# Kernel tuning notes

Hardware: AMD Instinct MI355X
Metric: run time of the kernel (lower is better)

## Reference

```python
import jax, jax.numpy as jnp
import numpy as np

B, T, C = 2, 4096, 768
H = 12
D = C // H  # head_dim = 64


def setup_inputs() -> dict:
    key = jax.random.key(0)
    k1, k2, k3 = jax.random.split(key, 3)
    x = jax.random.normal(k1, (B, T, C), dtype=jnp.float32)
    Wqkv = jax.random.normal(k2, (C, 3 * C), dtype=jnp.float32) * (C ** -0.5)
    Wproj = jax.random.normal(k3, (C, C), dtype=jnp.float32) * (C ** -0.5)
    bproj = jnp.zeros((C,), dtype=jnp.float32)
    return {"x": x, "Wqkv": Wqkv, "Wproj": Wproj, "bproj": bproj}


def reference(x, Wqkv, Wproj, bproj):
    b, t, c = x.shape
    # qkv projection (no bias), split into heads: [3, B, H, T, D]
    qkv = (x @ Wqkv).reshape(b, t, 3, H, D).transpose(2, 0, 3, 1, 4)
    q, k, v = qkv[0], qkv[1], qkv[2]
    scale = D ** -0.5
    # full causal score matrix [B, H, T, T] (faithful to naive impl)
    scores = jnp.einsum('bhqd,bhkd->bhqk', q, k) * scale
    causal = jnp.tril(jnp.ones((t, t), dtype=bool))
    scores = jnp.where(causal[None, None], scores, -jnp.inf)
    attn = jax.nn.softmax(scores, axis=-1)
    out = jnp.einsum('bhqk,bhkd->bhqd', attn, v)
    out = out.transpose(0, 2, 1, 3).reshape(b, t, c)
    return out @ Wproj + bproj
```

## Files before the change

kernel.cpp:

```cpp
#include <hip/hip_runtime.h>

#define B_ 2
#define T_ 4096
#define C_ 768
#define H_ 12
#define D_ 64
#define QTASK 96

typedef __attribute__((ext_vector_type(8))) short bf16x8;
typedef __attribute__((ext_vector_type(4))) float f32x4;
typedef __attribute__((ext_vector_type(16))) float f32x16;

__device__ __forceinline__ unsigned short f2bf(float f) {
  union { float f; unsigned u; } v; v.f = f;
  unsigned r = v.u + 0x7fffu + ((v.u >> 16) & 1u);
  return (unsigned short)(r >> 16);
}

__device__ __forceinline__ float exp2_hw(float x) {
  float r;
  asm("v_exp_f32 %0, %1" : "=v"(r) : "v"(x));
  return r;
}

__device__ __forceinline__ void gll16(const void* g, void* l) {
  __builtin_amdgcn_global_load_lds((const __attribute__((address_space(1))) void*)g,
                                   (__attribute__((address_space(3))) void*)l, 16, 0, 0);
}


__global__ __launch_bounds__(256) void cast_bf16_k(const float* __restrict__ in,
                                                   unsigned short* __restrict__ out, int n4,
                                                   unsigned* __restrict__ cnt) {
  int i = blockIdx.x * 256 + threadIdx.x;
  if (i < 128) cnt[i] = 0u;
  if (i >= n4) return;
  float4 v = ((const float4*)in)[i];
  union { unsigned short s[4]; unsigned long long u; } o;
  o.s[0] = f2bf(v.x); o.s[1] = f2bf(v.y); o.s[2] = f2bf(v.z); o.s[3] = f2bf(v.w);
  ((unsigned long long*)out)[i] = o.u;
}

__global__ __launch_bounds__(256) void tpose2_k(const float* __restrict__ a,
                                                unsigned short* __restrict__ ao,
                                                const float* __restrict__ b,
                                                unsigned short* __restrict__ bo) {
  __shared__ unsigned short t[64][65];
  int id = blockIdx.x;
  const float* in; unsigned short* out; int R, C, bx, by;
  if (id < 432) { in = a; out = ao; R = 768; C = 2304; bx = id % 36; by = id / 36; }
  else { id -= 432; in = b; out = bo; R = 768; C = 768; bx = id % 12; by = id / 12; }
  const int c0 = bx * 64, r0 = by * 64;
  const int tr = threadIdx.x >> 6, tc = threadIdx.x & 63;
#pragma unroll
  for (int i = 0; i < 16; ++i) {
    int r = i * 4 + tr;
    t[r][tc] = f2bf(in[(size_t)(r0 + r) * C + c0 + tc]);
  }
  __syncthreads();
#pragma unroll
  for (int i = 0; i < 16; ++i) {
    int c = i * 4 + tr;
    out[(size_t)(c0 + c) * R + r0 + tc] = t[tc][c];
  }
}


#define QSCALE 0.1803368801111243f

__global__ __launch_bounds__(256) void gemm_k(const unsigned short* __restrict__ A,
                                              const unsigned short* __restrict__ Bt,
                                              int K,
                                              unsigned short* __restrict__ q_out,
                                              unsigned short* __restrict__ k_out,
                                              unsigned short* __restrict__ vt_out) {
  __shared__ short a_lds[2][128 * 32];
  __shared__ short b_lds[2][128 * 32];
  const int tid = threadIdx.x;
  const int wave = tid >> 6, lane = tid & 63;
  const int wm = wave >> 1, wn = wave & 1;
  const int lr = lane & 15, lc = lane >> 4;

  const int id = blockIdx.x;
  const int xcd = id & 7, idc = id >> 3;
  const int bx = xcd * 8 + (idc & 7);
  const int by = idc >> 3;
  const int m0 = bx * 128, n0 = by * 128;

  f32x4 acc[4][4];
  for (int mi = 0; mi < 4; ++mi)
    for (int ni = 0; ni < 4; ++ni) acc[mi][ni] = (f32x4){0.f, 0.f, 0.f, 0.f};

  const unsigned short *ap[2], *bp[2];
  int lb[2];
#pragma unroll
  for (int p = 0; p < 2; ++p) {
    int chunk = p * 256 + wave * 64 + lane;
    int r = chunk >> 2, cc = chunk & 3;
    int c = cc ^ ((r >> 1) & 3);
    ap[p] = A + (size_t)(m0 + r) * K + c * 8;
    bp[p] = Bt + (size_t)(n0 + r) * K + c * 8;
    lb[p] = (p * 256 + wave * 64) * 8;
  }

  const int nks = K >> 5;
#pragma unroll
  for (int p = 0; p < 2; ++p) {
    gll16(ap[p], &a_lds[0][lb[p]]);
    gll16(bp[p], &b_lds[0][lb[p]]);
    ap[p] += 32; bp[p] += 32;
  }

  for (int ks = 0; ks < nks; ++ks) {
    const int buf = ks & 1;
    __builtin_amdgcn_s_barrier();
    __builtin_amdgcn_sched_barrier(0);
    if (ks + 1 < nks) {
#pragma unroll
      for (int p = 0; p < 2; ++p) {
        gll16(ap[p], &a_lds[buf ^ 1][lb[p]]);
        gll16(bp[p], &b_lds[buf ^ 1][lb[p]]);
        ap[p] += 32; bp[p] += 32;
      }
      asm volatile("s_waitcnt vmcnt(4)" ::: "memory");
    } else {
      asm volatile("s_waitcnt vmcnt(0)" ::: "memory");
    }
    __builtin_amdgcn_sched_barrier(0);
    __builtin_amdgcn_s_barrier();
    __builtin_amdgcn_sched_barrier(0);

    bf16x8 af[4], bfrag[4];
#pragma unroll
    for (int mi = 0; mi < 4; ++mi) {
      int r = wm * 64 + mi * 16 + lr;
      af[mi] = *(const bf16x8*)&a_lds[buf][r * 32 + (lc ^ ((r >> 1) & 3)) * 8];
    }
#pragma unroll
    for (int ni = 0; ni < 4; ++ni) {
      int r = wn * 64 + ni * 16 + lr;
      bfrag[ni] = *(const bf16x8*)&b_lds[buf][r * 32 + (lc ^ ((r >> 1) & 3)) * 8];
    }
    __builtin_amdgcn_s_setprio(1);
#pragma unroll
    for (int mi = 0; mi < 4; ++mi)
#pragma unroll
      for (int ni = 0; ni < 4; ++ni)
        acc[mi][ni] = __builtin_amdgcn_mfma_f32_16x16x32_bf16(af[mi], bfrag[ni], acc[mi][ni], 0, 0, 0);
    __builtin_amdgcn_s_setprio(0);
  }

  const int nn0 = n0 + wn * 64 + lr;
  const int which = n0 / 768;
#pragma unroll
  for (int mi = 0; mi < 4; ++mi)
#pragma unroll
    for (int ni = 0; ni < 4; ++ni) {
      int nn = nn0 + ni * 16;
      int rem = nn - which * 768;
      int h = rem >> 6, d = rem & 63;
      int t0v = m0 + wm * 64 + mi * 16 + lc * 4;
      int b = t0v >> 12, t = t0v & (T_ - 1);
      size_t bh = (size_t)(b * H_ + h);
      if (which == 2) {
        unsigned u0, u1;
        asm("v_cvt_pk_bf16_f32 %0, %1, %2" : "=v"(u0) : "v"(acc[mi][ni][0]), "v"(acc[mi][ni][1]));
        asm("v_cvt_pk_bf16_f32 %0, %1, %2" : "=v"(u1) : "v"(acc[mi][ni][2]), "v"(acc[mi][ni][3]));
        uint2 u = {u0, u1};
        *(uint2*)&vt_out[(bh * D_ + d) * T_ + t] = u;
      } else {
#pragma unroll
        for (int r = 0; r < 4; ++r) {
          float av = acc[mi][ni][r];
          if (which == 0) av *= QSCALE;
          unsigned short val = f2bf(av);
          if (which == 0) q_out[(bh * T_ + t + r) * D_ + d] = val;
          else            k_out[(bh * T_ + t + r) * D_ + d] = val;
        }
      }
    }
}


__global__ __launch_bounds__(256) void gemm2_k(const unsigned short* __restrict__ A,
                                               const unsigned short* __restrict__ Bt,
                                               float* __restrict__ f_out,
                                               const float* __restrict__ bias) {
  __shared__ short a_lds[2][64 * 32];
  __shared__ short b_lds[2][128 * 32];
  const int tid = threadIdx.x;
  const int wave = tid >> 6, lane = tid & 63;
  const int wm = wave >> 1, wn = wave & 1;
  const int lr = lane & 15, lc = lane >> 4;
  const int K = C_;

  const int id = blockIdx.x;
  const int xcd = id & 7, idc = id >> 3;
  const int bx = xcd * 16 + (idc & 15);
  const int by = idc >> 4;
  const int m0 = bx * 64, n0 = by * 128;

  f32x4 acc[2][4];
  for (int mi = 0; mi < 2; ++mi)
    for (int ni = 0; ni < 4; ++ni) acc[mi][ni] = (f32x4){0.f, 0.f, 0.f, 0.f};

  const unsigned short *apt, *bpt[2];
  int lba, lbb[2];
  {
    int chunk = wave * 64 + lane;
    int r = chunk >> 2, cc = chunk & 3;
    int c = cc ^ ((r >> 1) & 3);
    apt = A + (size_t)(m0 + r) * K + c * 8;
    lba = (wave * 64) * 8;
  }
#pragma unroll
  for (int p = 0; p < 2; ++p) {
    int chunk = p * 256 + wave * 64 + lane;
    int r = chunk >> 2, cc = chunk & 3;
    int c = cc ^ ((r >> 1) & 3);
    bpt[p] = Bt + (size_t)(n0 + r) * K + c * 8;
    lbb[p] = (p * 256 + wave * 64) * 8;
  }

  const int nks = K >> 5;
  gll16(apt, &a_lds[0][lba]); apt += 32;
#pragma unroll
  for (int p = 0; p < 2; ++p) { gll16(bpt[p], &b_lds[0][lbb[p]]); bpt[p] += 32; }

  for (int ks = 0; ks < nks; ++ks) {
    const int buf = ks & 1;
    __builtin_amdgcn_s_barrier();
    __builtin_amdgcn_sched_barrier(0);
    if (ks + 1 < nks) {
      gll16(apt, &a_lds[buf ^ 1][lba]); apt += 32;
#pragma unroll
      for (int p = 0; p < 2; ++p) { gll16(bpt[p], &b_lds[buf ^ 1][lbb[p]]); bpt[p] += 32; }
      asm volatile("s_waitcnt vmcnt(3)" ::: "memory");
    } else {
      asm volatile("s_waitcnt vmcnt(0)" ::: "memory");
    }
    __builtin_amdgcn_sched_barrier(0);
    __builtin_amdgcn_s_barrier();
    __builtin_amdgcn_sched_barrier(0);

    bf16x8 af[2], bfrag[4];
#pragma unroll
    for (int mi = 0; mi < 2; ++mi) {
      int r = wm * 32 + mi * 16 + lr;
      af[mi] = *(const bf16x8*)&a_lds[buf][r * 32 + (lc ^ ((r >> 1) & 3)) * 8];
    }
#pragma unroll
    for (int ni = 0; ni < 4; ++ni) {
      int r = wn * 64 + ni * 16 + lr;
      bfrag[ni] = *(const bf16x8*)&b_lds[buf][r * 32 + (lc ^ ((r >> 1) & 3)) * 8];
    }
    __builtin_amdgcn_s_setprio(1);
#pragma unroll
    for (int mi = 0; mi < 2; ++mi)
#pragma unroll
      for (int ni = 0; ni < 4; ++ni)
        acc[mi][ni] = __builtin_amdgcn_mfma_f32_16x16x32_bf16(af[mi], bfrag[ni], acc[mi][ni], 0, 0, 0);
    __builtin_amdgcn_s_setprio(0);
  }

#pragma unroll
  for (int mi = 0; mi < 2; ++mi)
#pragma unroll
    for (int ni = 0; ni < 4; ++ni) {
      int nn = n0 + wn * 64 + ni * 16 + lr;
      float bv = bias[nn];
#pragma unroll
      for (int r = 0; r < 4; ++r) {
        int m = m0 + wm * 32 + mi * 16 + lc * 4 + r;
        f_out[(size_t)m * C_ + nn] = acc[mi][ni][r] + bv;
      }
    }
}


#define PACK8(SV, O)                                                              \
  do {                                                                            \
    unsigned w0, w1, w2, w3, w4, w5, w6, w7;                                      \
    asm("v_cvt_pk_bf16_f32 %0, %1, %2" : "=v"(w0) : "v"(SV[0]), "v"(SV[1]));      \
    asm("v_cvt_pk_bf16_f32 %0, %1, %2" : "=v"(w1) : "v"(SV[2]), "v"(SV[3]));      \
    asm("v_cvt_pk_bf16_f32 %0, %1, %2" : "=v"(w2) : "v"(SV[4]), "v"(SV[5]));      \
    asm("v_cvt_pk_bf16_f32 %0, %1, %2" : "=v"(w3) : "v"(SV[6]), "v"(SV[7]));      \
    asm("v_cvt_pk_bf16_f32 %0, %1, %2" : "=v"(w4) : "v"(SV[8]), "v"(SV[9]));      \
    asm("v_cvt_pk_bf16_f32 %0, %1, %2" : "=v"(w5) : "v"(SV[10]), "v"(SV[11]));    \
    asm("v_cvt_pk_bf16_f32 %0, %1, %2" : "=v"(w6) : "v"(SV[12]), "v"(SV[13]));    \
    asm("v_cvt_pk_bf16_f32 %0, %1, %2" : "=v"(w7) : "v"(SV[14]), "v"(SV[15]));    \
    asm("v_permlane32_swap_b32 %0, %1" : "+v"(w0), "+v"(w2));                     \
    asm("v_permlane32_swap_b32 %0, %1" : "+v"(w1), "+v"(w3));                     \
    asm("v_permlane32_swap_b32 %0, %1" : "+v"(w4), "+v"(w6));                     \
    asm("v_permlane32_swap_b32 %0, %1" : "+v"(w5), "+v"(w7));                     \
    pw[(O) + 0] = w0; pw[(O) + 1] = w1; pw[(O) + 2] = w2; pw[(O) + 3] = w3;       \
    pw[(O) + 4] = w4; pw[(O) + 5] = w5; pw[(O) + 6] = w6; pw[(O) + 7] = w7;       \
  } while (0)

__global__ __launch_bounds__(256) void flash5_k(const unsigned short* __restrict__ Qg,
                                                const unsigned short* __restrict__ Kg,
                                                const unsigned short* __restrict__ Vtg,
                                                unsigned short* __restrict__ Og,
                                                unsigned* __restrict__ cnt) {
  __shared__ short k_lds[2][8 * 512];
  __shared__ short vt_lds[2][8 * 512];
  __shared__ int task_s;

  const int tid = threadIdx.x;
  const int wave = tid >> 6, lane = tid & 63;
  const int lq = lane & 31, hi = lane >> 5;
  const int xq = blockIdx.x & 7;
  unsigned* myq = cnt + xq * 16;

  for (;;) {
    if (tid == 0) task_s = (int)atomicAdd(myq, 1u);
    __syncthreads();
    const int task = task_s;
    if (task >= QTASK) return;

    const int qi = 31 - task / 3;
    const int bh = xq * 3 + (task - (task / 3) * 3);
    const int qw = qi * 128 + wave * 32;
    const int q_g = qw + lq;

    const size_t kbase = (size_t)bh * T_ * D_;
    const size_t vbase = (size_t)bh * D_ * T_;

    const unsigned short* qrow = Qg + kbase + (size_t)q_g * D_;
    bf16x8 qf[4];
#pragma unroll
    for (int t = 0; t < 4; ++t) qf[t] = *(const bf16x8*)(qrow + t * 16 + hi * 8);

    f32x16 accT0, accT1;
#pragma unroll
    for (int r = 0; r < 16; ++r) { accT0[r] = 0.f; accT1[r] = 0.f; }
    float lvec[16];
#pragma unroll
    for (int r = 0; r < 16; ++r) lvec[r] = 0.f;
    float m = 0.f;

    const int nt = 2 * qi + 2;

    const unsigned short* kp = Kg + kbase + (size_t)((wave & 1) * 32 + lq) * D_ + (wave >> 1) * 16 + hi * 8;
    const unsigned short* vp = Vtg + vbase + (size_t)((wave & 1) * 32 + lq) * T_ + (wave >> 1) * 16 + hi * 8;
    const int lb0 = wave * 512, lb1 = (wave + 4) * 512;

    gll16(kp, &k_lds[0][lb0]); gll16(kp + 32, &k_lds[0][lb1]);
    gll16(vp, &vt_lds[0][lb0]); gll16(vp + 32, &vt_lds[0][lb1]);
    const unsigned short* kpn = kp + 64 * D_;
    const unsigned short* vpn = vp + 64;

    for (int it = 0; it < nt; ++it) {
      const int kv = it * 64;
      const int buf = it & 1;

      __builtin_amdgcn_s_barrier();
      __builtin_amdgcn_sched_barrier(0);
      if (it + 1 < nt) {
        gll16(kpn, &k_lds[buf ^ 1][lb0]); gll16(kpn + 32, &k_lds[buf ^ 1][lb1]);
        gll16(vpn, &vt_lds[buf ^ 1][lb0]); gll16(vpn + 32, &vt_lds[buf ^ 1][lb1]);
        kpn += 64 * D_; vpn += 64;
        asm volatile("s_waitcnt vmcnt(4)" ::: "memory");
      } else {
        asm volatile("s_waitcnt vmcnt(0)" ::: "memory");
      }
      __builtin_amdgcn_sched_barrier(0);
      __builtin_amdgcn_s_barrier();
      __builtin_amdgcn_sched_barrier(0);

      if (kv <= qw + 31) {
        const float negm = -m;
        f32x16 s0, s1;
#pragma unroll
        for (int r = 0; r < 16; ++r) { s0[r] = negm; s1[r] = negm; }
        __builtin_amdgcn_s_setprio(1);
#pragma unroll
        for (int t = 0; t < 4; ++t) {
          bf16x8 kf0 = *(const bf16x8*)&k_lds[buf][(t * 2 + 0) * 512 + lane * 8];
          bf16x8 kf1 = *(const bf16x8*)&k_lds[buf][(t * 2 + 1) * 512 + lane * 8];
          s0 = __builtin_amdgcn_mfma_f32_32x32x16_bf16(kf0, qf[t], s0, 0, 0, 0);
          s1 = __builtin_amdgcn_mfma_f32_32x32x16_bf16(kf1, qf[t], s1, 0, 0, 0);
        }
        __builtin_amdgcn_s_setprio(0);

        if (kv + 63 > qw) {
#pragma unroll
          for (int r = 0; r < 16; ++r) {
            int key0 = kv + ((r & 3) + 8 * (r >> 2) + 4 * hi);
            if (key0 > q_g) s0[r] = -INFINITY;
            if (key0 + 32 > q_g) s1[r] = -INFINITY;
          }
        }

        float mx[16];
#pragma unroll
        for (int r = 0; r < 16; ++r) mx[r] = fmaxf(s0[r], s1[r]);
        float a0 = fmaxf(fmaxf(mx[0], mx[1]), mx[2]);
        float a1 = fmaxf(fmaxf(mx[3], mx[4]), mx[5]);
        float a2 = fmaxf(fmaxf(mx[6], mx[7]), mx[8]);
        float a3 = fmaxf(fmaxf(mx[9], mx[10]), mx[11]);
        float a4 = fmaxf(fmaxf(mx[12], mx[13]), mx[14]);
        float rx = fmaxf(fmaxf(fmaxf(a0, a1), fmaxf(a2, a3)), fmaxf(a4, mx[15]));
        rx = fmaxf(rx, __shfl_xor(rx, 32));

        if (!__all(rx <= 8.f)) {
          float dlt = fmaxf(rx, 0.f);
          float al = exp2_hw(-dlt);
          m += dlt;
#pragma unroll
          for (int r = 0; r < 16; ++r) { accT0[r] *= al; accT1[r] *= al; lvec[r] *= al; }
#pragma unroll
          for (int r = 0; r < 16; ++r) { s0[r] -= dlt; s1[r] -= dlt; }
        }
#pragma unroll
        for (int r = 0; r < 16; ++r) s0[r] = exp2_hw(s0[r]);
#pragma unroll
        for (int r = 0; r < 16; ++r) s1[r] = exp2_hw(s1[r]);
#pragma unroll
        for (int r = 0; r < 16; ++r) lvec[r] += s0[r] + s1[r];

        unsigned pw[16];
        PACK8(s0, 0);
        PACK8(s1, 8);

        __builtin_amdgcn_s_setprio(1);
#pragma unroll
        for (int ks = 0; ks < 4; ++ks) {
          union { unsigned u[4]; bf16x8 v; } pb;
          pb.u[0] = pw[ks * 4 + 0]; pb.u[1] = pw[ks * 4 + 1];
          pb.u[2] = pw[ks * 4 + 2]; pb.u[3] = pw[ks * 4 + 3];
          bf16x8 vf0 = *(const bf16x8*)&vt_lds[buf][(ks * 2 + 0) * 512 + lane * 8];
          bf16x8 vf1 = *(const bf16x8*)&vt_lds[buf][(ks * 2 + 1) * 512 + lane * 8];
          accT0 = __builtin_amdgcn_mfma_f32_32x32x16_bf16(vf0, pb.v, accT0, 0, 0, 0);
          accT1 = __builtin_amdgcn_mfma_f32_32x32x16_bf16(vf1, pb.v, accT1, 0, 0, 0);
        }
        __builtin_amdgcn_s_setprio(0);
      }
    }

    float l = 0.f;
#pragma unroll
    for (int r = 0; r < 16; ++r) l += lvec[r];
    l += __shfl_xor(l, 32);
    const float inv = 1.0f / l;
    const int b = bh / H_, h = bh - b * H_;
    unsigned short* orow = Og + ((size_t)b * T_ + q_g) * C_ + h * D_;
#pragma unroll
    for (int g = 0; g < 4; ++g) {
      int d0 = 8 * g + 4 * hi;
      float e0 = accT0[4 * g + 0] * inv, e1 = accT0[4 * g + 1] * inv;
      float e2 = accT0[4 * g + 2] * inv, e3 = accT0[4 * g + 3] * inv;
      float f0 = accT1[4 * g + 0] * inv, f1 = accT1[4 * g + 1] * inv;
      float f2 = accT1[4 * g + 2] * inv, f3 = accT1[4 * g + 3] * inv;
      uint2 ua, ub;
      asm("v_cvt_pk_bf16_f32 %0, %1, %2" : "=v"(ua.x) : "v"(e0), "v"(e1));
      asm("v_cvt_pk_bf16_f32 %0, %1, %2" : "=v"(ua.y) : "v"(e2), "v"(e3));
      asm("v_cvt_pk_bf16_f32 %0, %1, %2" : "=v"(ub.x) : "v"(f0), "v"(f1));
      asm("v_cvt_pk_bf16_f32 %0, %1, %2" : "=v"(ub.y) : "v"(f2), "v"(f3));
      *(uint2*)(orow + d0) = ua;
      *(uint2*)(orow + 32 + d0) = ub;
    }
    __syncthreads();
  }
}


extern "C" void kernel_launch(void* const* d_in, const int* in_sizes, int n_in,
                              void* d_out, int out_size, void* d_ws, size_t ws_size,
                              hipStream_t stream) {
  const float* x     = (const float*)d_in[0];
  const float* Wqkv  = (const float*)d_in[1];
  const float* Wproj = (const float*)d_in[2];
  const float* bproj = (const float*)d_in[3];
  float* out = (float*)d_out;

  char* ws = (char*)d_ws;
  unsigned short* xbf   = (unsigned short*)(ws);
  unsigned short* wqkvt = (unsigned short*)(ws + 12582912);
  unsigned short* wprjt = (unsigned short*)(ws + 16121856);
  unsigned short* Qb    = (unsigned short*)(ws + 17301504);
  unsigned short* Kb    = (unsigned short*)(ws + 29884416);
  unsigned short* Vtb   = (unsigned short*)(ws + 42467328);
  unsigned*       cnt   = (unsigned*)(ws + 55050240);

  cast_bf16_k<<<6144, 256, 0, stream>>>(x, xbf, (B_ * T_ * C_) / 4, cnt);
  tpose2_k<<<576, 256, 0, stream>>>(Wqkv, wqkvt, Wproj, wprjt);

  gemm_k<<<(B_ * T_ / 128) * (3 * C_ / 128), 256, 0, stream>>>(
      xbf, wqkvt, C_, Qb, Kb, Vtb);

  flash5_k<<<1024, 256, 0, stream>>>(Qb, Kb, Vtb, xbf, cnt);

  gemm2_k<<<(B_ * T_ / 64) * (C_ / 128), 256, 0, stream>>>(xbf, wprjt, out, bproj);
}
```

Baseline: 194.1 us.

## Split long causal query tiles across KV halves with separate merge kernel

```diff
diff --git a/kernel.cpp b/kernel.cpp
--- a/kernel.cpp
+++ b/kernel.cpp
@@ -5,7 +5,7 @@
 #define C_ 768
 #define H_ 12
 #define D_ 64
-#define QTASK 96
+#define QTASK 144
 
 typedef __attribute__((ext_vector_type(8))) short bf16x8;
 typedef __attribute__((ext_vector_type(4))) float f32x4;
@@ -277,6 +277,25 @@
     }
 }
 
+__device__ const unsigned char g_tasktbl[48] = {
+  15, 0x80|31, 0xC0|31,
+      0x80|30, 0xC0|30,
+  14, 0x80|29, 0xC0|29,
+      0x80|28, 0xC0|28,
+  13, 0x80|27, 0xC0|27,
+      0x80|26, 0xC0|26,
+  12, 0x80|25, 0xC0|25,
+      0x80|24, 0xC0|24,
+  11, 0x80|23, 0xC0|23,
+      0x80|22, 0xC0|22,
+  10, 0x80|21, 0xC0|21,
+      0x80|20, 0xC0|20,
+   9, 0x80|19, 0xC0|19,
+      0x80|18, 0xC0|18,
+   8, 0x80|17, 0xC0|17,
+      0x80|16, 0xC0|16,
+   7, 6, 5, 4, 3, 2, 1, 0
+};
 
 #define PACK8(SV, O)                                                              \
   do {                                                                            \
@@ -297,11 +316,12 @@
     pw[(O) + 4] = w4; pw[(O) + 5] = w5; pw[(O) + 6] = w6; pw[(O) + 7] = w7;       \
   } while (0)
 
-__global__ __launch_bounds__(256) void flash5_k(const unsigned short* __restrict__ Qg,
-                                                const unsigned short* __restrict__ Kg,
-                                                const unsigned short* __restrict__ Vtg,
-                                                unsigned short* __restrict__ Og,
-                                                unsigned* __restrict__ cnt) {
+__global__ __launch_bounds__(256) void flash14_k(const unsigned short* __restrict__ Qg,
+                                                 const unsigned short* __restrict__ Kg,
+                                                 const unsigned short* __restrict__ Vtg,
+                                                 unsigned short* __restrict__ Og,
+                                                 unsigned* __restrict__ cnt,
+                                                 unsigned short* __restrict__ part) {
   __shared__ short k_lds[2][8 * 512];
   __shared__ short vt_lds[2][8 * 512];
   __shared__ int task_s;
@@ -318,11 +338,19 @@
     const int task = task_s;
     if (task >= QTASK) return;
 
-    const int qi = 31 - task / 3;
-    const int bh = xq * 3 + (task - (task / 3) * 3);
+    const int d3 = task / 3;
+    const int desc = g_tasktbl[d3];
+    const int qi = desc & 63;
+    const int split = desc >> 7;
+    const int half = (desc >> 6) & 1;
+    const int bh = xq * 3 + (task - d3 * 3);
     const int qw = qi * 128 + wave * 32;
     const int q_g = qw + lq;
 
+    const int it0 = (split && half) ? (qi + 1) : 0;
+    const int itN = split ? (half ? (2 * qi + 2) : (qi + 1)) : (2 * qi + 2);
+    const int ntl = itN - it0;
+
     const size_t kbase = (size_t)bh * T_ * D_;
     const size_t vbase = (size_t)bh * D_ * T_;
 
@@ -339,10 +367,10 @@
     for (int r = 0; r < 16; ++r) lvec[r] = 0.f;
     float m = 0.f;
 
-    const int nt = 2 * qi + 2;
-
-    const unsigned short* kp = Kg + kbase + (size_t)((wave & 1) * 32 + lq) * D_ + (wave >> 1) * 16 + hi * 8;
-    const unsigned short* vp = Vtg + vbase + (size_t)((wave & 1) * 32 + lq) * T_ + (wave >> 1) * 16 + hi * 8;
+    const unsigned short* kp = Kg + kbase + (size_t)((wave & 1) * 32 + lq) * D_ +
+                               (wave >> 1) * 16 + hi * 8 + (size_t)it0 * 64 * D_;
+    const unsigned short* vp = Vtg + vbase + (size_t)((wave & 1) * 32 + lq) * T_ +
+                               (wave >> 1) * 16 + hi * 8 + it0 * 64;
     const int lb0 = wave * 512, lb1 = (wave + 4) * 512;
 
     gll16(kp, &k_lds[0][lb0]); gll16(kp + 32, &k_lds[0][lb1]);
@@ -350,13 +378,13 @@
     const unsigned short* kpn = kp + 64 * D_;
     const unsigned short* vpn = vp + 64;
 
-    for (int it = 0; it < nt; ++it) {
-      const int kv = it * 64;
-      const int buf = it & 1;
+    for (int j = 0; j < ntl; ++j) {
+      const int kv = (it0 + j) * 64;
+      const int buf = j & 1;
 
       __builtin_amdgcn_s_barrier();
       __builtin_amdgcn_sched_barrier(0);
-      if (it + 1 < nt) {
+      if (j + 1 < ntl) {
         gll16(kpn, &k_lds[buf ^ 1][lb0]); gll16(kpn + 32, &k_lds[buf ^ 1][lb1]);
         gll16(vpn, &vt_lds[buf ^ 1][lb0]); gll16(vpn + 32, &vt_lds[buf ^ 1][lb1]);
         kpn += 64 * D_; vpn += 64;
@@ -442,25 +470,101 @@
 #pragma unroll
     for (int r = 0; r < 16; ++r) l += lvec[r];
     l += __shfl_xor(l, 32);
-    const float inv = 1.0f / l;
-    const int b = bh / H_, h = bh - b * H_;
-    unsigned short* orow = Og + ((size_t)b * T_ + q_g) * C_ + h * D_;
-#pragma unroll
-    for (int g = 0; g < 4; ++g) {
-      int d0 = 8 * g + 4 * hi;
-      float e0 = accT0[4 * g + 0] * inv, e1 = accT0[4 * g + 1] * inv;
-      float e2 = accT0[4 * g + 2] * inv, e3 = accT0[4 * g + 3] * inv;
-      float f0 = accT1[4 * g + 0] * inv, f1 = accT1[4 * g + 1] * inv;
-      float f2 = accT1[4 * g + 2] * inv, f3 = accT1[4 * g + 3] * inv;
-      uint2 ua, ub;
-      asm("v_cvt_pk_bf16_f32 %0, %1, %2" : "=v"(ua.x) : "v"(e0), "v"(e1));
-      asm("v_cvt_pk_bf16_f32 %0, %1, %2" : "=v"(ua.y) : "v"(e2), "v"(e3));
-      asm("v_cvt_pk_bf16_f32 %0, %1, %2" : "=v"(ub.x) : "v"(f0), "v"(f1));
-      asm("v_cvt_pk_bf16_f32 %0, %1, %2" : "=v"(ub.y) : "v"(f2), "v"(f3));
-      *(uint2*)(orow + d0) = ua;
-      *(uint2*)(orow + 32 + d0) = ub;
+
+    if (!split) {
+      const float inv = 1.0f / l;
+      const int b = bh / H_, h = bh - b * H_;
+      unsigned short* orow = Og + ((size_t)b * T_ + q_g) * C_ + h * D_;
+#pragma unroll
+      for (int g = 0; g < 4; ++g) {
+        int d0 = 8 * g + 4 * hi;
+        float e0 = accT0[4 * g + 0] * inv, e1 = accT0[4 * g + 1] * inv;
+        float e2 = accT0[4 * g + 2] * inv, e3 = accT0[4 * g + 3] * inv;
+        float f0 = accT1[4 * g + 0] * inv, f1 = accT1[4 * g + 1] * inv;
+        float f2 = accT1[4 * g + 2] * inv, f3 = accT1[4 * g + 3] * inv;
+        uint2 ua, ub;
+        asm("v_cvt_pk_bf16_f32 %0, %1, %2" : "=v"(ua.x) : "v"(e0), "v"(e1));
+        asm("v_cvt_pk_bf16_f32 %0, %1, %2" : "=v"(ua.y) : "v"(e2), "v"(e3));
+        asm("v_cvt_pk_bf16_f32 %0, %1, %2" : "=v"(ub.x) : "v"(f0), "v"(f1));
+        asm("v_cvt_pk_bf16_f32 %0, %1, %2" : "=v"(ub.y) : "v"(f2), "v"(f3));
+        *(uint2*)(orow + d0) = ua;
+        *(uint2*)(orow + 32 + d0) = ub;
+      }
+    } else {
+      unsigned short* pbase = part + (size_t)((bh * 16 + (qi - 16)) * 2 + half) * 9216;
+      unsigned w[16];
+#pragma unroll
+      for (int g = 0; g < 8; ++g)
+        asm("v_cvt_pk_bf16_f32 %0, %1, %2" : "=v"(w[g]) : "v"(accT0[2 * g]), "v"(accT0[2 * g + 1]));
+#pragma unroll
+      for (int g = 0; g < 8; ++g)
+        asm("v_cvt_pk_bf16_f32 %0, %1, %2" : "=v"(w[8 + g]) : "v"(accT1[2 * g]), "v"(accT1[2 * g + 1]));
+      uint4* po = (uint4*)(pbase + tid * 32);
+#pragma unroll
+      for (int g = 0; g < 4; ++g) {
+        uint4 u = {w[4 * g + 0], w[4 * g + 1], w[4 * g + 2], w[4 * g + 3]};
+        po[g] = u;
+      }
+      float2 ml = {m, l};
+      ((float2*)(pbase + 8192))[tid] = ml;
     }
     __syncthreads();
+  }
+}
+
+__global__ __launch_bounds__(256) void merge_k(const unsigned short* __restrict__ part,
+                                               unsigned short* __restrict__ Og) {
+  const int slot = blockIdx.x;
+  const int bh = slot >> 4, qi = (slot & 15) + 16;
+  const int tid = threadIdx.x;
+  const int wave = tid >> 6, lane = tid & 63;
+  const int lq = lane & 31, hi = lane >> 5;
+
+  const unsigned short* pa = part + (size_t)(slot * 2 + 0) * 9216;
+  const unsigned short* pb = part + (size_t)(slot * 2 + 1) * 9216;
+  float2 mla = ((const float2*)(pa + 8192))[tid];
+  float2 mlb = ((const float2*)(pb + 8192))[tid];
+  float newm = fmaxf(mla.x, mlb.x);
+  float sa = exp2_hw(mla.x - newm), sb = exp2_hw(mlb.x - newm);
+  float l = mla.y * sa + mlb.y * sb;
+  float inv = 1.0f / l;
+
+  const uint4* qa = (const uint4*)(pa + tid * 32);
+  const uint4* qb = (const uint4*)(pb + tid * 32);
+  float o[32];
+#pragma unroll
+  for (int g = 0; g < 4; ++g) {
+    uint4 ua = qa[g], ub = qb[g];
+#pragma unroll
+    for (int e = 0; e < 4; ++e) {
+      unsigned wa = ((const unsigned*)&ua)[e];
+      unsigned wb = ((const unsigned*)&ub)[e];
+      union { unsigned u; float f; } la_, ha_, lb_, hb_;
+      la_.u = wa << 16; ha_.u = wa & 0xffff0000u;
+      lb_.u = wb << 16; hb_.u = wb & 0xffff0000u;
+      int r = g * 8 + e * 2;
+      o[r]     = la_.f * sa + lb_.f * sb;
+      o[r + 1] = ha_.f * sa + hb_.f * sb;
+    }
+  }
+
+  const int q_g = qi * 128 + wave * 32 + lq;
+  const int b = bh / H_, h = bh - b * H_;
+  unsigned short* orow = Og + ((size_t)b * T_ + q_g) * C_ + h * D_;
+#pragma unroll
+  for (int g = 0; g < 4; ++g) {
+    int d0 = 8 * g + 4 * hi;
+    float e0 = o[4 * g + 0] * inv, e1 = o[4 * g + 1] * inv;
+    float e2 = o[4 * g + 2] * inv, e3 = o[4 * g + 3] * inv;
+    float f0 = o[16 + 4 * g + 0] * inv, f1 = o[16 + 4 * g + 1] * inv;
+    float f2 = o[16 + 4 * g + 2] * inv, f3 = o[16 + 4 * g + 3] * inv;
+    uint2 ua, ub;
+    asm("v_cvt_pk_bf16_f32 %0, %1, %2" : "=v"(ua.x) : "v"(e0), "v"(e1));
+    asm("v_cvt_pk_bf16_f32 %0, %1, %2" : "=v"(ua.y) : "v"(e2), "v"(e3));
+    asm("v_cvt_pk_bf16_f32 %0, %1, %2" : "=v"(ub.x) : "v"(f0), "v"(f1));
+    asm("v_cvt_pk_bf16_f32 %0, %1, %2" : "=v"(ub.y) : "v"(f2), "v"(f3));
+    *(uint2*)(orow + d0) = ua;
+    *(uint2*)(orow + 32 + d0) = ub;
   }
 }
 
@@ -482,6 +586,7 @@
   unsigned short* Kb    = (unsigned short*)(ws + 29884416);
   unsigned short* Vtb   = (unsigned short*)(ws + 42467328);
   unsigned*       cnt   = (unsigned*)(ws + 55050240);
+  unsigned short* part  = (unsigned short*)(ws + 55052288);
 
   cast_bf16_k<<<6144, 256, 0, stream>>>(x, xbf, (B_ * T_ * C_) / 4, cnt);
   tpose2_k<<<576, 256, 0, stream>>>(Wqkv, wqkvt, Wproj, wprjt);
@@ -489,7 +594,8 @@
   gemm_k<<<(B_ * T_ / 128) * (3 * C_ / 128), 256, 0, stream>>>(
       xbf, wqkvt, C_, Qb, Kb, Vtb);
 
-  flash5_k<<<1024, 256, 0, stream>>>(Qb, Kb, Vtb, xbf, cnt);
+  flash14_k<<<1024, 256, 0, stream>>>(Qb, Kb, Vtb, xbf, cnt, part);
+  merge_k<<<384, 256, 0, stream>>>(part, xbf);
 
   gemm2_k<<<(B_ * T_ / 64) * (C_ / 128), 256, 0, stream>>>(xbf, wprjt, out, bproj);
 }
```

Result: no change. 193.8 us (median of 2 runs) (-0.2%).
